# Performance work log

Hardware: AMD Instinct MI355X
Metric: run time of the kernel (lower is better)

Reference implementation:

```python
import jax, jax.numpy as jnp
import numpy as np

B, T, D = 4, 2048, 1024
E = 16            # routed experts
S = 2             # shared experts
MOE_TOPK = 2
COSINE_LAMBDA = 0.1


def setup_inputs() -> dict:
    key = jax.random.key(0)
    k_x, k_g, k_sh, k_rt = jax.random.split(key, 4)
    x = jax.random.normal(k_x, (B, T, D), dtype=jnp.float32)
    gate_w = jax.random.normal(k_g, (E, D), dtype=jnp.float32) * 0.02
    gate_b = jnp.zeros((E,), dtype=jnp.float32)
    shared_experts = jax.random.normal(k_sh, (S, D), dtype=jnp.float32) * 0.1
    routed_experts = jax.random.normal(k_rt, (E, D), dtype=jnp.float32) * 0.1
    return {"x": x, "gate_w": gate_w, "gate_b": gate_b,
            "shared_experts": shared_experts, "routed_experts": routed_experts}


def reference(x, gate_w, gate_b, shared_experts, routed_experts):
    b, t, d = x.shape
    n = b * t
    hidden = x.reshape(n, d)                                   # [N, D]

    # ---- router ----
    logits = hidden @ gate_w.T + gate_b                        # [N, E]
    probs = jax.nn.softmax(logits, axis=-1)                    # stable (shift-invariant)
    topk_vals, topk_idx = jax.lax.top_k(probs, MOE_TOPK)       # [N, K]
    if MOE_TOPK == 1:
        weights = jnp.ones_like(topk_vals)
    else:
        weights = topk_vals / jnp.clip(topk_vals.sum(-1, keepdims=True), 1e-6)

    # ---- shared experts (always active): sum_e hidden * w_e ----
    shared_sum = hidden * shared_experts.sum(0)                # [N, D]

    # ---- dense all-expert elementwise scale (as in original) ----
    routed_outs = hidden[None, :, :] * routed_experts[:, None, :]   # [E, N, D]

    # ---- diversity loss: cosine sim between flattened expert outputs ----
    flat = routed_outs.reshape(E, -1)                          # [E, N*D]
    norms = jnp.maximum(jnp.linalg.norm(flat, axis=1, keepdims=True), 1e-8)
    normed = flat / norms
    sim = jnp.clip(normed @ normed.T, -1.0, 1.0)               # [E, E]
    mask = 1.0 - jnp.eye(E, dtype=sim.dtype)
    div_loss = (sim * mask).sum() / max(E * (E - 1), 1) * COSINE_LAMBDA

    # ---- top-k gather + weighted combine ----
    routed_nd = routed_outs.transpose(1, 0, 2)                 # [N, E, D]
    sel = jnp.take_along_axis(routed_nd, topk_idx[:, :, None], axis=1)  # [N, K, D]
    dyn_sum = (sel * weights[:, :, None]).sum(axis=1)          # [N, D]

    out = (shared_sum + dyn_sum).reshape(b, t, d)
    return out, div_loss
```

## Files before the change

### kernel.cpp

```cpp
#include <hip/hip_runtime.h>

#define NTOK 8192
#define DDIM 1024
#define NEXP 16
#define NPAIR 136
#define NREP 8
#define XROW 1032

#define WS_GWT 0
#define WS_SG  16384
#define WS_GP  (16384 + NREP * DDIM)

__global__ __launch_bounds__(256) void moe_prep(
    const float* __restrict__ gate_w,
    float* __restrict__ ws)
{
    const int gid = blockIdx.x * 256 + threadIdx.x;
    const int e = gid & 15;
    const int d4 = gid >> 4;
    const float4* gw4 = (const float4*)gate_w;
    float4* gwT4 = (float4*)(ws + WS_GWT);
    gwT4[d4 * 16 + e] = gw4[e * 256 + d4];
    float* s_glob = ws + WS_SG;
    s_glob[gid] = 0.f;
    s_glob[gid + 4096] = 0.f;
}

__global__ __launch_bounds__(256, 4) void moe_fused(
    const float* __restrict__ x,
    const float* __restrict__ gate_b,
    const float* __restrict__ sh,
    const float* __restrict__ re,
    float* __restrict__ out,
    float* __restrict__ ws)
{
    __shared__ float xt[8][XROW];

    const int t = threadIdx.x;
    const int b = blockIdx.x;
    const float4* gwT4 = (const float4*)(ws + WS_GWT);
    float* s_glob = ws + WS_SG;

    float4 ss = make_float4(0.f, 0.f, 0.f, 0.f);
    {
        const float4* x4 = (const float4*)x + (size_t)b * 2048;
        #pragma unroll
        for (int i = 0; i < 8; ++i) {
            float4 v = x4[i * 256 + t];
            *(float4*)&xt[i][4 * t] = v;
            ss.x = fmaf(v.x, v.x, ss.x);
            ss.y = fmaf(v.y, v.y, ss.y);
            ss.z = fmaf(v.z, v.z, ss.z);
            ss.w = fmaf(v.w, v.w, ss.w);
        }
    }
    __syncthreads();

    const int lane = t & 63;
    const int wave = t >> 6;
    const int e = lane & 15;
    const int h = (lane >> 4) & 1;
    const int g = lane >> 5;

    const int tokL = wave * 2 + g;
    const float* xrow = &xt[tokL][h * 512];
    const float4* gt = gwT4 + h * 128 * 16;
    float4 a4 = make_float4(0.f, 0.f, 0.f, 0.f);
    #pragma unroll 8
    for (int i = 0; i < 128; ++i) {
        float4 xv = *(const float4*)(xrow + 4 * i);
        float4 gv = gt[i * 16 + e];
        a4.x = fmaf(xv.x, gv.x, a4.x);
        a4.y = fmaf(xv.y, gv.y, a4.y);
        a4.z = fmaf(xv.z, gv.z, a4.z);
        a4.w = fmaf(xv.w, gv.w, a4.w);
    }
    float acc = (a4.x + a4.y) + (a4.z + a4.w);
    acc += __shfl_xor(acc, 16, 64);
    acc += gate_b[e];

    float v0 = -3.0e38f, v1 = -3.0e38f;
    int i0 = 0, i1 = 0;
    const int base = lane & 32;
    #pragma unroll
    for (int j = 0; j < NEXP; ++j) {
        float lv = __shfl(acc, base + j, 64);
        if (lv > v0)      { v1 = v0; i1 = i0; v0 = lv; i0 = j; }
        else if (lv > v1) { v1 = lv; i1 = j; }
    }
    float ex = __expf(v1 - v0);
    float w0 = 1.f / (1.f + ex);
    float w1 = ex * w0;

    float4 shs[4];
    {
        const float4* s0 = (const float4*)sh;
        const float4* s1 = (const float4*)(sh + DDIM);
        #pragma unroll
        for (int j = 0; j < 4; ++j) {
            float4 p = s0[lane + 64 * j];
            float4 q = s1[lane + 64 * j];
            shs[j] = make_float4(p.x + q.x, p.y + q.y, p.z + q.z, p.w + q.w);
        }
    }

    #pragma unroll
    for (int tk = 0; tk < 2; ++tk) {
        const int src = tk << 5;
        float a0 = __shfl(w0, src, 64);
        float a1 = __shfl(w1, src, 64);
        int   e0 = __shfl(i0, src, 64);
        int   e1 = __shfl(i1, src, 64);
        const int tokL2 = wave * 2 + tk;
        const float4* xr = (const float4*)&xt[tokL2][0];
        const float4* r0 = (const float4*)(re + (size_t)e0 * DDIM);
        const float4* r1 = (const float4*)(re + (size_t)e1 * DDIM);
        float4* o = (float4*)(out + ((size_t)b * 8 + tokL2) * DDIM);
        #pragma unroll
        for (int j = 0; j < 4; ++j) {
            float4 xv = xr[lane + 64 * j];
            float4 b0 = r0[lane + 64 * j];
            float4 b1 = r1[lane + 64 * j];
            float4 r;
            r.x = xv.x * (shs[j].x + a0 * b0.x + a1 * b1.x);
            r.y = xv.y * (shs[j].y + a0 * b0.y + a1 * b1.y);
            r.z = xv.z * (shs[j].z + a0 * b0.z + a1 * b1.z);
            r.w = xv.w * (shs[j].w + a0 * b0.w + a1 * b1.w);
            o[lane + 64 * j] = r;
        }
    }

    {
        float* rep = s_glob + (size_t)(b & (NREP - 1)) * DDIM;
        atomicAdd(&rep[4 * t + 0], ss.x);
        atomicAdd(&rep[4 * t + 1], ss.y);
        atomicAdd(&rep[4 * t + 2], ss.z);
        atomicAdd(&rep[4 * t + 3], ss.w);
    }
}

__global__ __launch_bounds__(320) void moe_div_partial(
    const float* __restrict__ re,
    const float* __restrict__ ws,
    float* __restrict__ G_part_unused)
{
    __shared__ float reT[64][17];
    __shared__ float s4[4][64];
    __shared__ float s_loc[64];

    const int t = threadIdx.x;
    const int b = blockIdx.x;
    const int d0 = b * 64;
    const float* s_glob = ws + WS_SG;
    float* G_part = (float*)(ws + WS_GP);

    if (t < 256) {
        int c = t & 63, r = t >> 6;
        s4[r][c] = s_glob[r * DDIM + d0 + c] + s_glob[(r + 4) * DDIM + d0 + c];
        int e = t >> 4, d4 = t & 15;
        float4 v = ((const float4*)(re + (size_t)e * DDIM + d0))[d4];
        reT[d4 * 4 + 0][e] = v.x;
        reT[d4 * 4 + 1][e] = v.y;
        reT[d4 * 4 + 2][e] = v.z;
        reT[d4 * 4 + 3][e] = v.w;
    }
    __syncthreads();
    if (t < 64) s_loc[t] = (s4[0][t] + s4[1][t]) + (s4[2][t] + s4[3][t]);
    __syncthreads();

    const int p = t >> 1;
    const int half = t & 1;
    float a = 0.f;
    int pe = 0, pf = 0;
    if (p < NPAIR) {
        int rem = p;
        while (rem >= NEXP - pe) { rem -= NEXP - pe; ++pe; }
        pf = pe + rem;
        #pragma unroll
        for (int i = 0; i < 32; ++i) {
            int dd = half * 32 + i;
            a += s_loc[dd] * reT[dd][pe] * reT[dd][pf];
        }
    }
    a += __shfl_down(a, 1, 64);
    if (p < NPAIR && half == 0) G_part[b * NPAIR + p] = a;
}

__global__ __launch_bounds__(192) void moe_div_final(
    const float* __restrict__ ws,
    float* __restrict__ div_out)
{
    __shared__ float G[NPAIR];
    __shared__ float nr[NEXP];
    __shared__ float lsum;
    const float* G_part = ws + WS_GP;
    const int t = threadIdx.x;

    if (t == 0) lsum = 0.f;
    if (t < NPAIR) {
        float g = 0.f;
        #pragma unroll
        for (int b = 0; b < 16; ++b) g += G_part[b * NPAIR + t];
        G[t] = g;
    }
    __syncthreads();
    if (t < NEXP) {
        int idx = t * NEXP - (t * (t - 1)) / 2;
        nr[t] = fmaxf(sqrtf(G[idx]), 1e-8f);
    }
    __syncthreads();
    if (t < NPAIR) {
        int pe = 0, rem = t;
        while (rem >= NEXP - pe) { rem -= NEXP - pe; ++pe; }
        int pf = pe + rem;
        if (pe != pf) {
            float sim = G[t] / (nr[pe] * nr[pf]);
            sim = fminf(1.f, fmaxf(-1.f, sim));
            atomicAdd(&lsum, 2.f * sim);
        }
    }
    __syncthreads();
    if (t == 0) *div_out = lsum / (float)(NEXP * (NEXP - 1)) * 0.1f;
}

extern "C" void kernel_launch(void* const* d_in, const int* in_sizes, int n_in,
                              void* d_out, int out_size, void* d_ws, size_t ws_size,
                              hipStream_t stream) {
    const float* x  = (const float*)d_in[0];
    const float* gw = (const float*)d_in[1];
    const float* gb = (const float*)d_in[2];
    const float* sh = (const float*)d_in[3];
    const float* re = (const float*)d_in[4];
    float* out = (float*)d_out;
    float* ws = (float*)d_ws;

    moe_prep<<<16, 256, 0, stream>>>(gw, ws);
    moe_fused<<<1024, 256, 0, stream>>>(x, gb, sh, re, out, ws);
    moe_div_partial<<<16, 320, 0, stream>>>(re, ws, nullptr);
    moe_div_final<<<1, 192, 0, stream>>>(ws, out + (size_t)NTOK * DDIM);
}
```

Baseline: 124.6 us.

## Stage gate weights in LDS, read x from global, reduce sum-of-squares per block

The fused kernel now runs 512 threads over 16 tokens per block. It copies the full transposed gate matrix (64 KB) into LDS instead of staging x rows, and reads x directly from global memory for both the router dot products and the output pass. Per-dimension sum-of-squares is accumulated in the output loop, reduced in LDS with shared atomics, then flushed once per block to global. This cuts global atomics and gate-weight global reads, but adds a 64 KB LDS fill per block that limits occupancy, and x is read from global twice.

```diff
diff --git a/kernel.cpp b/kernel.cpp
--- a/kernel.cpp
+++ b/kernel.cpp
@@ -5,7 +5,6 @@
 #define NEXP 16
 #define NPAIR 136
 #define NREP 8
-#define XROW 1032
 
 #define WS_GWT 0
 #define WS_SG  16384
@@ -26,7 +25,7 @@
     s_glob[gid + 4096] = 0.f;
 }
 
-__global__ __launch_bounds__(256, 4) void moe_fused(
+__global__ __launch_bounds__(512, 4) void moe_fused(
     const float* __restrict__ x,
     const float* __restrict__ gate_b,
     const float* __restrict__ sh,
@@ -34,25 +33,19 @@
     float* __restrict__ out,
     float* __restrict__ ws)
 {
-    __shared__ float xt[8][XROW];
+    __shared__ float gwl[NEXP * DDIM];
+    __shared__ float s_part[DDIM];
 
     const int t = threadIdx.x;
     const int b = blockIdx.x;
-    const float4* gwT4 = (const float4*)(ws + WS_GWT);
-    float* s_glob = ws + WS_SG;
-
-    float4 ss = make_float4(0.f, 0.f, 0.f, 0.f);
+
     {
-        const float4* x4 = (const float4*)x + (size_t)b * 2048;
-        #pragma unroll
-        for (int i = 0; i < 8; ++i) {
-            float4 v = x4[i * 256 + t];
-            *(float4*)&xt[i][4 * t] = v;
-            ss.x = fmaf(v.x, v.x, ss.x);
-            ss.y = fmaf(v.y, v.y, ss.y);
-            ss.z = fmaf(v.z, v.z, ss.z);
-            ss.w = fmaf(v.w, v.w, ss.w);
-        }
+        const float4* src = (const float4*)(ws + WS_GWT);
+        float4* dst = (float4*)gwl;
+        #pragma unroll
+        for (int k = 0; k < 8; ++k) dst[t + k * 512] = src[t + k * 512];
+        s_part[t] = 0.f;
+        s_part[t + 512] = 0.f;
     }
     __syncthreads();
 
@@ -61,15 +54,15 @@
     const int e = lane & 15;
     const int h = (lane >> 4) & 1;
     const int g = lane >> 5;
-
-    const int tokL = wave * 2 + g;
-    const float* xrow = &xt[tokL][h * 512];
-    const float4* gt = gwT4 + h * 128 * 16;
+    const int n0 = b * 16 + wave * 2;
+
+    const float4* xr = (const float4*)(x + (size_t)(n0 + g) * DDIM) + h * 128;
+    const float4* gl = (const float4*)gwl + (size_t)h * 128 * 16 + e;
     float4 a4 = make_float4(0.f, 0.f, 0.f, 0.f);
     #pragma unroll 8
     for (int i = 0; i < 128; ++i) {
-        float4 xv = *(const float4*)(xrow + 4 * i);
-        float4 gv = gt[i * 16 + e];
+        float4 xv = xr[i];
+        float4 gv = gl[i * 16];
         a4.x = fmaf(xv.x, gv.x, a4.x);
         a4.y = fmaf(xv.y, gv.y, a4.y);
         a4.z = fmaf(xv.z, gv.z, a4.z);
@@ -103,6 +96,10 @@
             shs[j] = make_float4(p.x + q.x, p.y + q.y, p.z + q.z, p.w + q.w);
         }
     }
+
+    float4 ss[4];
+    #pragma unroll
+    for (int j = 0; j < 4; ++j) ss[j] = make_float4(0.f, 0.f, 0.f, 0.f);
 
     #pragma unroll
     for (int tk = 0; tk < 2; ++tk) {
@@ -111,14 +108,13 @@
         float a1 = __shfl(w1, src, 64);
         int   e0 = __shfl(i0, src, 64);
         int   e1 = __shfl(i1, src, 64);
-        const int tokL2 = wave * 2 + tk;
-        const float4* xr = (const float4*)&xt[tokL2][0];
+        const float4* xrow = (const float4*)(x + (size_t)(n0 + tk) * DDIM);
         const float4* r0 = (const float4*)(re + (size_t)e0 * DDIM);
         const float4* r1 = (const float4*)(re + (size_t)e1 * DDIM);
-        float4* o = (float4*)(out + ((size_t)b * 8 + tokL2) * DDIM);
+        float4* o = (float4*)(out + (size_t)(n0 + tk) * DDIM);
         #pragma unroll
         for (int j = 0; j < 4; ++j) {
-            float4 xv = xr[lane + 64 * j];
+            float4 xv = xrow[lane + 64 * j];
             float4 b0 = r0[lane + 64 * j];
             float4 b1 = r1[lane + 64 * j];
             float4 r;
@@ -127,22 +123,35 @@
             r.z = xv.z * (shs[j].z + a0 * b0.z + a1 * b1.z);
             r.w = xv.w * (shs[j].w + a0 * b0.w + a1 * b1.w);
             o[lane + 64 * j] = r;
-        }
-    }
-
-    {
-        float* rep = s_glob + (size_t)(b & (NREP - 1)) * DDIM;
-        atomicAdd(&rep[4 * t + 0], ss.x);
-        atomicAdd(&rep[4 * t + 1], ss.y);
-        atomicAdd(&rep[4 * t + 2], ss.z);
-        atomicAdd(&rep[4 * t + 3], ss.w);
+            ss[j].x = fmaf(xv.x, xv.x, ss[j].x);
+            ss[j].y = fmaf(xv.y, xv.y, ss[j].y);
+            ss[j].z = fmaf(xv.z, xv.z, ss[j].z);
+            ss[j].w = fmaf(xv.w, xv.w, ss[j].w);
+        }
+    }
+
+    #pragma unroll
+    for (int j = 0; j < 4; ++j) {
+        int d = 4 * (lane + 64 * j);
+        atomicAdd(&s_part[d + 0], ss[j].x);
+        atomicAdd(&s_part[d + 1], ss[j].y);
+        atomicAdd(&s_part[d + 2], ss[j].z);
+        atomicAdd(&s_part[d + 3], ss[j].w);
+    }
+    __syncthreads();
+    if (t < 256) {
+        float* rep = ws + WS_SG + (size_t)(b & (NREP - 1)) * DDIM;
+        float4 v = ((float4*)s_part)[t];
+        atomicAdd(&rep[4 * t + 0], v.x);
+        atomicAdd(&rep[4 * t + 1], v.y);
+        atomicAdd(&rep[4 * t + 2], v.z);
+        atomicAdd(&rep[4 * t + 3], v.w);
     }
 }
 
 __global__ __launch_bounds__(320) void moe_div_partial(
     const float* __restrict__ re,
-    const float* __restrict__ ws,
-    float* __restrict__ G_part_unused)
+    float* __restrict__ ws)
 {
     __shared__ float reT[64][17];
     __shared__ float s4[4][64];
@@ -152,7 +161,7 @@
     const int b = blockIdx.x;
     const int d0 = b * 64;
     const float* s_glob = ws + WS_SG;
-    float* G_part = (float*)(ws + WS_GP);
+    float* G_part = ws + WS_GP;
 
     if (t < 256) {
         int c = t & 63, r = t >> 6;
@@ -171,11 +180,10 @@
     const int p = t >> 1;
     const int half = t & 1;
     float a = 0.f;
-    int pe = 0, pf = 0;
     if (p < NPAIR) {
-        int rem = p;
+        int pe = 0, rem = p;
         while (rem >= NEXP - pe) { rem -= NEXP - pe; ++pe; }
-        pf = pe + rem;
+        int pf = pe + rem;
         #pragma unroll
         for (int i = 0; i < 32; ++i) {
             int dd = half * 32 + i;
@@ -235,7 +243,7 @@
     float* ws = (float*)d_ws;
 
     moe_prep<<<16, 256, 0, stream>>>(gw, ws);
-    moe_fused<<<1024, 256, 0, stream>>>(x, gb, sh, re, out, ws);
-    moe_div_partial<<<16, 320, 0, stream>>>(re, ws, nullptr);
+    moe_fused<<<512, 512, 0, stream>>>(x, gb, sh, re, out, ws);
+    moe_div_partial<<<16, 320, 0, stream>>>(re, ws);
     moe_div_final<<<1, 192, 0, stream>>>(ws, out + (size_t)NTOK * DDIM);
 }
```

Measured after the change: 135.6 us. +8.8%, slower.

## Split fused MoE kernel into routing and separate high-occupancy combine kernel

Applied to the files above, without the earlier changes.

The fused router/combine kernel is split in two. A routing kernel writes per-token top-2 weights and indices to the workspace. A new combine kernel, with one wave per token and higher occupancy, rereads x from global memory and writes the output with nontemporal stores. This aims to free the combine phase from the LDS-limited occupancy of the routing kernel, at the cost of an extra kernel launch and a second pass over x.

```diff
diff --git a/kernel.cpp b/kernel.cpp
--- a/kernel.cpp
+++ b/kernel.cpp
@@ -7,9 +7,12 @@
 #define NREP 8
 #define XROW 1032
 
+typedef float vfloat4 __attribute__((ext_vector_type(4)));
+
 #define WS_GWT 0
 #define WS_SG  16384
 #define WS_GP  (16384 + NREP * DDIM)
+#define WS_RT  (16384 + NREP * DDIM + 16 * NPAIR)
 
 __global__ __launch_bounds__(256) void moe_prep(
     const float* __restrict__ gate_w,
@@ -26,12 +29,9 @@
     s_glob[gid + 4096] = 0.f;
 }
 
-__global__ __launch_bounds__(256, 4) void moe_fused(
+__global__ __launch_bounds__(256, 4) void moe_route(
     const float* __restrict__ x,
     const float* __restrict__ gate_b,
-    const float* __restrict__ sh,
-    const float* __restrict__ re,
-    float* __restrict__ out,
     float* __restrict__ ws)
 {
     __shared__ float xt[8][XROW];
@@ -40,6 +40,7 @@
     const int b = blockIdx.x;
     const float4* gwT4 = (const float4*)(ws + WS_GWT);
     float* s_glob = ws + WS_SG;
+    float4* route = (float4*)(ws + WS_RT);
 
     float4 ss = make_float4(0.f, 0.f, 0.f, 0.f);
     {
@@ -92,43 +93,9 @@
     float w0 = 1.f / (1.f + ex);
     float w1 = ex * w0;
 
-    float4 shs[4];
-    {
-        const float4* s0 = (const float4*)sh;
-        const float4* s1 = (const float4*)(sh + DDIM);
-        #pragma unroll
-        for (int j = 0; j < 4; ++j) {
-            float4 p = s0[lane + 64 * j];
-            float4 q = s1[lane + 64 * j];
-            shs[j] = make_float4(p.x + q.x, p.y + q.y, p.z + q.z, p.w + q.w);
-        }
-    }
-
-    #pragma unroll
-    for (int tk = 0; tk < 2; ++tk) {
-        const int src = tk << 5;
-        float a0 = __shfl(w0, src, 64);
-        float a1 = __shfl(w1, src, 64);
-        int   e0 = __shfl(i0, src, 64);
-        int   e1 = __shfl(i1, src, 64);
-        const int tokL2 = wave * 2 + tk;
-        const float4* xr = (const float4*)&xt[tokL2][0];
-        const float4* r0 = (const float4*)(re + (size_t)e0 * DDIM);
-        const float4* r1 = (const float4*)(re + (size_t)e1 * DDIM);
-        float4* o = (float4*)(out + ((size_t)b * 8 + tokL2) * DDIM);
-        #pragma unroll
-        for (int j = 0; j < 4; ++j) {
-            float4 xv = xr[lane + 64 * j];
-            float4 b0 = r0[lane + 64 * j];
-            float4 b1 = r1[lane + 64 * j];
-            float4 r;
-            r.x = xv.x * (shs[j].x + a0 * b0.x + a1 * b1.x);
-            r.y = xv.y * (shs[j].y + a0 * b0.y + a1 * b1.y);
-            r.z = xv.z * (shs[j].z + a0 * b0.z + a1 * b1.z);
-            r.w = xv.w * (shs[j].w + a0 * b0.w + a1 * b1.w);
-            o[lane + 64 * j] = r;
-        }
-    }
+    if ((lane & 31) == 0)
+        route[b * 8 + tokL] =
+            make_float4(w0, w1, __int_as_float(i0), __int_as_float(i1));
 
     {
         float* rep = s_glob + (size_t)(b & (NREP - 1)) * DDIM;
@@ -139,10 +106,50 @@
     }
 }
 
+__global__ __launch_bounds__(256, 8) void moe_combine(
+    const float* __restrict__ x,
+    const float* __restrict__ sh,
+    const float* __restrict__ re,
+    const float* __restrict__ ws,
+    float* __restrict__ out)
+{
+    const int t = threadIdx.x;
+    const int lane = t & 63;
+    const int n = blockIdx.x * 4 + (t >> 6);
+    const float4* route = (const float4*)(ws + WS_RT);
+
+    float4 rec = route[n];
+    const float a0 = rec.x, a1 = rec.y;
+    const int e0 = __float_as_int(rec.z);
+    const int e1 = __float_as_int(rec.w);
+
+    const float4* s0 = (const float4*)sh;
+    const float4* s1 = (const float4*)(sh + DDIM);
+    const float4* xr = (const float4*)(x + (size_t)n * DDIM);
+    const float4* r0 = (const float4*)(re + (size_t)e0 * DDIM);
+    const float4* r1 = (const float4*)(re + (size_t)e1 * DDIM);
+    vfloat4* o = (vfloat4*)(out + (size_t)n * DDIM);
+
+    #pragma unroll
+    for (int j = 0; j < 4; ++j) {
+        const int idx = lane + 64 * j;
+        float4 xv = xr[idx];
+        float4 p  = s0[idx];
+        float4 q  = s1[idx];
+        float4 b0 = r0[idx];
+        float4 b1 = r1[idx];
+        vfloat4 r;
+        r.x = xv.x * ((p.x + q.x) + a0 * b0.x + a1 * b1.x);
+        r.y = xv.y * ((p.y + q.y) + a0 * b0.y + a1 * b1.y);
+        r.z = xv.z * ((p.z + q.z) + a0 * b0.z + a1 * b1.z);
+        r.w = xv.w * ((p.w + q.w) + a0 * b0.w + a1 * b1.w);
+        __builtin_nontemporal_store(r, &o[idx]);
+    }
+}
+
 __global__ __launch_bounds__(320) void moe_div_partial(
     const float* __restrict__ re,
-    const float* __restrict__ ws,
-    float* __restrict__ G_part_unused)
+    float* __restrict__ ws)
 {
     __shared__ float reT[64][17];
     __shared__ float s4[4][64];
@@ -152,7 +159,7 @@
     const int b = blockIdx.x;
     const int d0 = b * 64;
     const float* s_glob = ws + WS_SG;
-    float* G_part = (float*)(ws + WS_GP);
+    float* G_part = ws + WS_GP;
 
     if (t < 256) {
         int c = t & 63, r = t >> 6;
@@ -171,11 +178,10 @@
     const int p = t >> 1;
     const int half = t & 1;
     float a = 0.f;
-    int pe = 0, pf = 0;
     if (p < NPAIR) {
-        int rem = p;
+        int pe = 0, rem = p;
         while (rem >= NEXP - pe) { rem -= NEXP - pe; ++pe; }
-        pf = pe + rem;
+        int pf = pe + rem;
         #pragma unroll
         for (int i = 0; i < 32; ++i) {
             int dd = half * 32 + i;
@@ -235,7 +241,8 @@
     float* ws = (float*)d_ws;
 
     moe_prep<<<16, 256, 0, stream>>>(gw, ws);
-    moe_fused<<<1024, 256, 0, stream>>>(x, gb, sh, re, out, ws);
-    moe_div_partial<<<16, 320, 0, stream>>>(re, ws, nullptr);
+    moe_route<<<1024, 256, 0, stream>>>(x, gb, ws);
+    moe_combine<<<2048, 256, 0, stream>>>(x, sh, re, ws, out);
+    moe_div_partial<<<16, 320, 0, stream>>>(re, ws);
     moe_div_final<<<1, 192, 0, stream>>>(ws, out + (size_t)NTOK * DDIM);
 }
```

Result: slower. 154.5 us (+24.0%).
